# Performance work log

Hardware: AMD Instinct MI355X
Metric: run time of the kernel (lower is better)

Reference implementation:

```python
import jax, jax.numpy as jnp
import numpy as np

B, L, H, HD, FD = 1, 1024, 32, 64, 64
HID = H * HD
EPS = 1e-12


def setup_inputs() -> dict:
    key = jax.random.key(0)
    ks = jax.random.split(key, 7)
    s = 1.0 / np.sqrt(HID)
    return {
        "hidden_states": jax.random.normal(ks[0], (B, L, HID), dtype=jnp.float32),
        "Wq": jax.random.normal(ks[1], (HID, HID), dtype=jnp.float32) * s,
        "Wk": jax.random.normal(ks[2], (HID, HID), dtype=jnp.float32) * s,
        "Wv": jax.random.normal(ks[3], (HID, HID), dtype=jnp.float32) * s,
        "Wo": jax.random.normal(ks[4], (HID, HID), dtype=jnp.float32) * s,
        "Wfq": jax.random.normal(ks[5], (H, HD, FD), dtype=jnp.float32) * (1.0 / np.sqrt(HD)),
        "Wfk": jax.random.normal(ks[6], (H, HD, FD), dtype=jnp.float32) * (1.0 / np.sqrt(HD)),
    }


def _heads(x):
    # [b, l, hid] -> [b, h, l, hd]
    b, l, _ = x.shape
    return x.reshape(b, l, H, HD).transpose(0, 2, 1, 3)


def _feature_map(x, Wf):
    # per-head learned kernel + softmax over feature dim (hedgehog-style)
    z = jnp.einsum('bhld,hdf->bhlf', x, Wf)
    return jax.nn.softmax(z, axis=-1)


def _linear_attention(q, k, v, eps=EPS):
    # causal_dot_product: cumsum of outer-product KV state (fp32)
    qf, kf, vf = q.astype(jnp.float32), k.astype(jnp.float32), v.astype(jnp.float32)
    kv = jnp.cumsum(jnp.einsum('bhlf,bhld->bhlfd', kf, vf), axis=2)  # [b,h,l,f,d]
    y = jnp.einsum('bhlf,bhlfd->bhld', qf, kv)
    # fp32_attention=False branch: normalizer computed on cumsum(k)
    k_cum = jnp.cumsum(kf, axis=2).astype(q.dtype)
    denom = jnp.einsum('bhld,bhld->bhl', q, k_cum) + eps
    return y.astype(q.dtype) / denom[..., None]


def reference(hidden_states, Wq, Wk, Wv, Wo, Wfq, Wfk):
    b, l, _ = hidden_states.shape
    q = _heads(hidden_states @ Wq.T)
    k = _heads(hidden_states @ Wk.T)
    v = _heads(hidden_states @ Wv.T)
    fq = _feature_map(q, Wfq)
    fk = _feature_map(k, Wfk)
    y = _linear_attention(fq, fk, v)  # [b,h,l,hd]
    y = y.transpose(0, 2, 1, 3).reshape(b, l, HID)
    return y @ Wo.T
```

## Files before the change

kernel.cpp:

```cpp
#include <hip/hip_runtime.h>
#include <math.h>

constexpr int LQ  = 1024;
constexpr int NH  = 32;
constexpr int HDM = 64;
constexpr int FDM = 64;
constexpr int HID = 2048;
constexpr int NCH = 16;
constexpr int CT  = 64;
#define EPSV 1e-12f

typedef __bf16 bf16x8 __attribute__((ext_vector_type(8)));
typedef float  f32x4  __attribute__((ext_vector_type(4)));

__device__ __forceinline__ unsigned short f2b_raw(float x) {
    union { float f; unsigned int u; } v; v.f = x;
    unsigned int r = v.u + 0x7fffu + ((v.u >> 16) & 1u);
    return (unsigned short)(r >> 16);
}
__device__ __forceinline__ float b2f(ushort u) {
    union { unsigned int i; float f; } v; v.i = ((unsigned int)u) << 16; return v.f;
}

#define ASYNC16(ldsp, gp) __builtin_amdgcn_global_load_lds( \
    (const __attribute__((address_space(1))) void*)(gp),    \
    (__attribute__((address_space(3))) void*)(ldsp), 16, 0, 0)

template <int TM, int TN, bool BF16OUT>
__device__ __forceinline__ void gemm_core(const ushort* __restrict__ A,
                                          const ushort* __restrict__ B,
                                          void* __restrict__ Cv,
                                          int M, int N, int K) {
    constexpr int FI = TM / 32, FJ = TN / 32;
    constexpr int AI = TM / 32, BJ = TN / 32;
    constexpr int ASZ = TM * 64, BSZ = TN * 64;
    __shared__ __align__(16) ushort As[2 * ASZ];
    __shared__ __align__(16) ushort Bs[2 * BSZ];

    const int t = threadIdx.x, wave = t >> 6, lane = t & 63;
    const int wr = (wave >> 1) * (TM / 2), wc = (wave & 1) * (TN / 2);
    const int bm = blockIdx.y * TM, bn = blockIdx.x * TN;

    const int grow = lane >> 3;
    const int gsw  = ((lane & 7) ^ (grow & 7)) << 3;
    const int arow0 = wave * (TM / 4), brow0 = wave * (TN / 4);
    const ushort* gA = A + (size_t)(bm + arow0 + grow) * K + gsw;
    const ushort* gB = B + (size_t)(bn + brow0 + grow) * K + gsw;

    const int fr = lane & 15, q = lane >> 4;

    f32x4 acc[FI][FJ] = {};
    const int NIT = K >> 6;

    {
        ushort* ab = As + arow0 * 64;
        ushort* bb = Bs + brow0 * 64;
#pragma unroll
        for (int i = 0; i < AI; ++i) ASYNC16(ab + i * 512, gA + (size_t)i * 8 * K);
#pragma unroll
        for (int j = 0; j < BJ; ++j) ASYNC16(bb + j * 512, gB + (size_t)j * 8 * K);
    }
    __syncthreads();

    for (int it = 0; it < NIT; ++it) {
        const int p = it & 1;
        if (it + 1 < NIT) {
            const int ko = (it + 1) << 6;
            ushort* ab = As + (p ^ 1) * ASZ + arow0 * 64;
            ushort* bb = Bs + (p ^ 1) * BSZ + brow0 * 64;
#pragma unroll
            for (int i = 0; i < AI; ++i) ASYNC16(ab + i * 512, gA + ko + (size_t)i * 8 * K);
#pragma unroll
            for (int j = 0; j < BJ; ++j) ASYNC16(bb + j * 512, gB + ko + (size_t)j * 8 * K);
        }
        const ushort* ap = As + p * ASZ;
        const ushort* bp = Bs + p * BSZ;
        bf16x8 af[2][FI], bg[2][FJ];
#pragma unroll
        for (int ks = 0; ks < 2; ++ks) {
#pragma unroll
            for (int i = 0; i < FI; ++i) {
                const int row = wr + i * 16 + fr;
                af[ks][i] = *(const bf16x8*)&ap[row * 64 + (((q + ks * 4) ^ (row & 7)) << 3)];
            }
#pragma unroll
            for (int j = 0; j < FJ; ++j) {
                const int row = wc + j * 16 + fr;
                bg[ks][j] = *(const bf16x8*)&bp[row * 64 + (((q + ks * 4) ^ (row & 7)) << 3)];
            }
        }
#pragma unroll
        for (int ks = 0; ks < 2; ++ks)
#pragma unroll
            for (int i = 0; i < FI; ++i)
#pragma unroll
                for (int j = 0; j < FJ; ++j)
                    acc[i][j] = __builtin_amdgcn_mfma_f32_16x16x32_bf16(af[ks][i], bg[ks][j], acc[i][j], 0, 0, 0);
        if (it + 1 < NIT) __syncthreads();
    }

    const int er = q * 4, ec = lane & 15;
#pragma unroll
    for (int i = 0; i < FI; ++i)
#pragma unroll
        for (int j = 0; j < FJ; ++j) {
            const size_t base = (size_t)(bm + wr + i * 16 + er) * N + bn + wc + j * 16 + ec;
            if constexpr (BF16OUT) {
                ushort* C = (ushort*)Cv;
#pragma unroll
                for (int r = 0; r < 4; ++r) C[base + (size_t)r * N] = f2b_raw(acc[i][j][r]);
            } else {
                float* C = (float*)Cv;
#pragma unroll
                for (int r = 0; r < 4; ++r) C[base + (size_t)r * N] = acc[i][j][r];
            }
        }
}

__global__ __launch_bounds__(256) void gemm_one(const ushort* __restrict__ A,
                                                const ushort* __restrict__ B,
                                                float* __restrict__ C) {
    gemm_core<64, 64, false>(A, B, C, LQ, HID, HID);
}

__global__ __launch_bounds__(256) void gemm_qkv_fm(
    const ushort* __restrict__ hsb,
    const ushort* __restrict__ wqb, const ushort* __restrict__ wkb,
    const ushort* __restrict__ wvb,
    const ushort* __restrict__ WfqT, const ushort* __restrict__ WfkT,
    ushort* __restrict__ fqB, ushort* __restrict__ fkB,
    ushort* __restrict__ VTb) {
    constexpr int TM = 64, TN = 128;
    constexpr int ASZ = TM * 64, BSZ = TN * 64;
    __shared__ __align__(16) ushort lds[2 * ASZ + 2 * BSZ];
    ushort* As = lds;
    ushort* Bs = lds + 2 * ASZ;

    const int z = blockIdx.z;
    const ushort* Bmat = (z == 0) ? wqb : (z == 1) ? wkb : wvb;

    const int t = threadIdx.x, wave = t >> 6, lane = t & 63;
    const int wr = (wave >> 1) * 32, wc = (wave & 1) * 64;
    const int bx = blockIdx.x, c = blockIdx.y;
    const int bm = c * TM, bn = bx * TN, l0 = c * CT;

    const int grow = lane >> 3;
    const int gsw  = ((lane & 7) ^ (grow & 7)) << 3;
    const int arow0 = wave * 16, brow0 = wave * 32;
    const ushort* gA = hsb  + (size_t)(bm + arow0 + grow) * HID + gsw;
    const ushort* gB = Bmat + (size_t)(bn + brow0 + grow) * HID + gsw;

    const int fr = lane & 15, q = lane >> 4, ec = lane & 15;

    f32x4 acc[2][4] = {};
    const int NIT = HID >> 6;

    {
        ushort* ab = As + arow0 * 64;
        ushort* bb = Bs + brow0 * 64;
#pragma unroll
        for (int i = 0; i < 2; ++i) ASYNC16(ab + i * 512, gA + (size_t)i * 8 * HID);
#pragma unroll
        for (int j = 0; j < 4; ++j) ASYNC16(bb + j * 512, gB + (size_t)j * 8 * HID);
    }
    __syncthreads();

    for (int it = 0; it < NIT; ++it) {
        const int p = it & 1;
        if (it + 1 < NIT) {
            const int ko = (it + 1) << 6;
            ushort* ab = As + (p ^ 1) * ASZ + arow0 * 64;
            ushort* bb = Bs + (p ^ 1) * BSZ + brow0 * 64;
#pragma unroll
            for (int i = 0; i < 2; ++i) ASYNC16(ab + i * 512, gA + ko + (size_t)i * 8 * HID);
#pragma unroll
            for (int j = 0; j < 4; ++j) ASYNC16(bb + j * 512, gB + ko + (size_t)j * 8 * HID);
        }
        const ushort* ap = As + p * ASZ;
        const ushort* bp = Bs + p * BSZ;
        bf16x8 af[2][2], bg[2][4];
#pragma unroll
        for (int ks = 0; ks < 2; ++ks) {
#pragma unroll
            for (int i = 0; i < 2; ++i) {
                const int row = wr + i * 16 + fr;
                af[ks][i] = *(const bf16x8*)&ap[row * 64 + (((q + ks * 4) ^ (row & 7)) << 3)];
            }
#pragma unroll
            for (int j = 0; j < 4; ++j) {
                const int row = wc + j * 16 + fr;
                bg[ks][j] = *(const bf16x8*)&bp[row * 64 + (((q + ks * 4) ^ (row & 7)) << 3)];
            }
        }
#pragma unroll
        for (int ks = 0; ks < 2; ++ks)
#pragma unroll
            for (int i = 0; i < 2; ++i)
#pragma unroll
                for (int j = 0; j < 4; ++j)
                    acc[i][j] = __builtin_amdgcn_mfma_f32_16x16x32_bf16(af[ks][i], bg[ks][j], acc[i][j], 0, 0, 0);
        if (it + 1 < NIT) __syncthreads();
    }

    if (z == 2) {
#pragma unroll
        for (int i = 0; i < 2; ++i)
#pragma unroll
            for (int j = 0; j < 4; ++j) {
                const int col = wc + j * 16 + ec;
                const int hh = col >> 6, d = col & 63;
                const int lb = wr + i * 16 + q * 4;
                const size_t base = (((size_t)(2 * bx + hh) * NCH + c) * 64 + d) * 64 + lb;
                ushort4 o = make_ushort4(f2b_raw(acc[i][j][0]), f2b_raw(acc[i][j][1]),
                                         f2b_raw(acc[i][j][2]), f2b_raw(acc[i][j][3]));
                *(ushort4*)&VTb[base] = o;
            }
        return;
    }

    __syncthreads();
    ushort* Qt  = lds;
    ushort* Wfs = lds + 8704;
#pragma unroll
    for (int i = 0; i < 2; ++i)
#pragma unroll
        for (int j = 0; j < 4; ++j)
#pragma unroll
            for (int r = 0; r < 4; ++r)
                Qt[(wr + i * 16 + q * 4 + r) * 136 + wc + j * 16 + ec] = f2b_raw(acc[i][j][r]);
    {
        const ushort* WT = ((z == 0) ? WfqT : WfkT) + (size_t)(2 * bx) * 4096;
#pragma unroll
        for (int it = 0; it < 4; ++it) {
            const int e = it * 2048 + t * 8;
            const int hh = e >> 12, f = (e >> 6) & 63, dc = e & 63;
            uint4 wv4 = *(const uint4*)&WT[e];
            *(uint4*)&Wfs[hh * 4608 + f * 72 + dc] = wv4;
        }
    }
    __syncthreads();

    const int hh = wave & 1, R0 = (wave >> 1) * 32;
    f32x4 z2[2][4] = {};
#pragma unroll
    for (int ks = 0; ks < 2; ++ks) {
        bf16x8 a[2];
#pragma unroll
        for (int i = 0; i < 2; ++i)
            a[i] = *(const bf16x8*)&Qt[(R0 + i * 16 + fr) * 136 + hh * 64 + ks * 32 + q * 8];
#pragma unroll
        for (int j = 0; j < 4; ++j) {
            bf16x8 b = *(const bf16x8*)&Wfs[hh * 4608 + (j * 16 + fr) * 72 + ks * 32 + q * 8];
#pragma unroll
            for (int i = 0; i < 2; ++i)
                z2[i][j] = __builtin_amdgcn_mfma_f32_16x16x32_bf16(a[i], b, z2[i][j], 0, 0, 0);
        }
    }

    ushort* outp = (z == 0) ? fqB : fkB;
    const int hgl = 2 * bx + hh;
#pragma unroll
    for (int i = 0; i < 2; ++i)
#pragma unroll
        for (int r = 0; r < 4; ++r) {
            float m = z2[i][0][r];
#pragma unroll
            for (int j = 1; j < 4; ++j) m = fmaxf(m, z2[i][j][r]);
            m = fmaxf(m, __shfl_xor(m, 1)); m = fmaxf(m, __shfl_xor(m, 2));
            m = fmaxf(m, __shfl_xor(m, 4)); m = fmaxf(m, __shfl_xor(m, 8));
            float e4[4], s = 0.f;
#pragma unroll
            for (int j = 0; j < 4; ++j) { e4[j] = __expf(z2[i][j][r] - m); s += e4[j]; }
            s += __shfl_xor(s, 1); s += __shfl_xor(s, 2);
            s += __shfl_xor(s, 4); s += __shfl_xor(s, 8);
            const float inv = 1.0f / s;
            const int l = R0 + i * 16 + q * 4 + r;
            ushort* op = outp + ((size_t)hgl * LQ + l0 + l) * FDM;
#pragma unroll
            for (int j = 0; j < 4; ++j) op[j * 16 + ec] = f2b_raw(e4[j] * inv);
        }
}

struct ConvArgs {
    const float* src[5]; ushort* dst[5]; int n[5];
    const float* Wfq; const float* Wfk; ushort* WfqT; ushort* WfkT;
};
__global__ __launch_bounds__(256) void conv_all(ConvArgs p) {
    const int y = blockIdx.y, t = threadIdx.x;
    if (y < 5) {
        const int i = (blockIdx.x * 256 + t) * 4;
        if (i >= p.n[y]) return;
        float4 v = *(const float4*)&p.src[y][i];
        ushort4 o = make_ushort4(f2b_raw(v.x), f2b_raw(v.y), f2b_raw(v.z), f2b_raw(v.w));
        *(ushort4*)&p.dst[y][i] = o;
        return;
    }
    if (blockIdx.x >= NH) return;
    const int h = blockIdx.x;
    const float* src = ((y == 6) ? p.Wfk : p.Wfq) + (size_t)h * 4096;
    ushort* dst = ((y == 6) ? p.WfkT : p.WfqT) + (size_t)h * 4096;
    __shared__ float tile[64][65];
    for (int it = 0; it < 16; ++it) {
        int e = it * 256 + t; int d = e >> 6, f = e & 63;
        tile[d][f] = src[e];
    }
    __syncthreads();
    for (int it = 0; it < 16; ++it) {
        int e = it * 256 + t; int f = e >> 6, d = e & 63;
        dst[e] = f2b_raw(tile[d][f]);
    }
}

__global__ __launch_bounds__(256) void chunk_state(
    const ushort* __restrict__ fkB, const ushort* __restrict__ VTb,
    float* __restrict__ Sraw, float* __restrict__ Ks) {
    __shared__ __align__(16) ushort Vs[64 * 72];
    __shared__ __align__(16) ushort Fs[64 * 72];
    const int c = blockIdx.x, h = blockIdx.y;
    const int t = threadIdx.x, lane = t & 63, w = t >> 6;
    const int l0 = c * CT;
    const int fr = lane & 15, q = lane >> 4, ec = lane & 15;
    const size_t cb = ((size_t)h * NCH + c) * 4096;

    for (int it = 0; it < 2; ++it) {
        const int e = (it * 256 + t) * 8;
        const int row = e >> 6, col = e & 63;
        *(uint4*)&Vs[row * 72 + col] = *(const uint4*)&VTb[cb + e];
        uint4 fv = *(const uint4*)&fkB[((size_t)h * LQ + l0) * FDM + e];
        const ushort* pf = (const ushort*)&fv;
#pragma unroll
        for (int i2 = 0; i2 < 8; ++i2) Fs[(col + i2) * 72 + row] = pf[i2];
    }
    __syncthreads();

    f32x4 acc[4] = {};
#pragma unroll
    for (int ks = 0; ks < 2; ++ks) {
        bf16x8 a = *(const bf16x8*)&Vs[(w * 16 + fr) * 72 + ks * 32 + q * 8];
#pragma unroll
        for (int j = 0; j < 4; ++j) {
            bf16x8 b = *(const bf16x8*)&Fs[(j * 16 + fr) * 72 + ks * 32 + q * 8];
            acc[j] = __builtin_amdgcn_mfma_f32_16x16x32_bf16(a, b, acc[j], 0, 0, 0);
        }
    }
    float* sp = Sraw + cb;
#pragma unroll
    for (int j = 0; j < 4; ++j)
#pragma unroll
        for (int r = 0; r < 4; ++r)
            sp[(w * 16 + q * 4 + r) * 64 + j * 16 + ec] = acc[j][r];
    if (t < 64) {
        float s = 0.f;
#pragma unroll 8
        for (int l = 0; l < 64; ++l) s += b2f(Fs[t * 72 + l]);
        Ks[((size_t)h * NCH + c) * FDM + t] = s;
    }
}

__global__ __launch_bounds__(256) void prefix2(const float* __restrict__ Sraw,
                                               ushort* __restrict__ SpreB,
                                               const float* __restrict__ Ks,
                                               float* __restrict__ Kpre) {
    const int h = blockIdx.x, eb = blockIdx.y, t = threadIdx.x;
    const int e0 = eb * 512 + t * 2;
    float r0 = 0.f, r1 = 0.f;
    const size_t hb = (size_t)h * NCH * 4096;
    for (int c2 = 0; c2 < NCH; ++c2) {
        const size_t base = hb + (size_t)c2 * 4096 + e0;
        float c0 = Sraw[base], c1 = Sraw[base + 1];
        ushort2 o = make_ushort2(f2b_raw(r0), f2b_raw(r1));
        *(ushort2*)&SpreB[base] = o;
        r0 += c0; r1 += c1;
    }
    if (eb == 0 && t < 64) {
        float rk = 0.f;
        for (int c2 = 0; c2 < NCH; ++c2) {
            const size_t kb2 = ((size_t)h * NCH + c2) * FDM + t;
            float cur = Ks[kb2];
            Kpre[kb2] = rk;
            rk += cur;
        }
    }
}

__global__ __launch_bounds__(256) void intra2(
    const ushort* __restrict__ fqB, const ushort* __restrict__ fkB,
    const ushort* __restrict__ VTb, const ushort* __restrict__ SpreB,
    const float* __restrict__ Kpre, ushort* __restrict__ Yb) {
    __shared__ __align__(16) ushort fqs[64 * 72];
    __shared__ __align__(16) ushort fks[64 * 72];
    __shared__ __align__(16) ushort VTs[64 * 72];
    __shared__ __align__(16) ushort Sps[64 * 72];
    __shared__ __align__(16) ushort Pms[64 * 72];
    __shared__ float den[64], kpr[64];

    const int c = blockIdx.x, h = blockIdx.y;
    const int t = threadIdx.x, lane = t & 63, wave = t >> 6;
    const int l0 = c * CT;
    const int fr = lane & 15, fo = (lane >> 4) * 8;
    const int g = lane >> 4, cc = lane & 15;

    const size_t qkbase = ((size_t)h * LQ + l0) * FDM;
    const size_t cbase  = ((size_t)h * NCH + c) * 4096;
    for (int it = 0; it < 2; ++it) {
        int e = (it * 256 + t) * 8;
        int row = e >> 6, col = e & 63;
        *(uint4*)&fqs[row * 72 + col] = *(const uint4*)&fqB[qkbase + e];
        *(uint4*)&fks[row * 72 + col] = *(const uint4*)&fkB[qkbase + e];
        *(uint4*)&VTs[row * 72 + col] = *(const uint4*)&VTb[cbase + e];
        *(uint4*)&Sps[row * 72 + col] = *(const uint4*)&SpreB[cbase + e];
    }
    if (t < 64) kpr[t] = Kpre[((size_t)h * NCH + c) * FDM + t];
    __syncthreads();

    f32x4 accP[4] = {};
#pragma unroll
    for (int kp = 0; kp < 2; ++kp) {
        bf16x8 a = *(const bf16x8*)&fqs[(wave * 16 + fr) * 72 + kp * 32 + fo];
#pragma unroll
        for (int j = 0; j < 4; ++j) {
            bf16x8 b = *(const bf16x8*)&fks[(j * 16 + fr) * 72 + kp * 32 + fo];
            accP[j] = __builtin_amdgcn_mfma_f32_16x16x32_bf16(a, b, accP[j], 0, 0, 0);
        }
    }
#pragma unroll
    for (int j = 0; j < 4; ++j)
#pragma unroll
        for (int r = 0; r < 4; ++r) {
            int l = wave * 16 + g * 4 + r, lp = j * 16 + cc;
            Pms[l * 72 + lp] = (lp <= l) ? f2b_raw(accP[j][r]) : (ushort)0;
        }
    __syncthreads();

    {
        const int srow = t >> 2, spart = t & 3;
        float s = 0.f;
#pragma unroll
        for (int i = 0; i < 16; ++i) s += b2f(Pms[srow * 72 + spart * 16 + i]);
#pragma unroll
        for (int i = 0; i < 16; ++i) s += b2f(fqs[srow * 72 + spart * 16 + i]) * kpr[spart * 16 + i];
        s += __shfl_xor(s, 1); s += __shfl_xor(s, 2);
        if (spart == 0) den[srow] = s + EPSV;
    }
    __syncthreads();

    f32x4 accY[4] = {};
#pragma unroll
    for (int kp = 0; kp < 2; ++kp) {
        bf16x8 a = *(const bf16x8*)&Pms[(wave * 16 + fr) * 72 + kp * 32 + fo];
#pragma unroll
        for (int j = 0; j < 4; ++j) {
            bf16x8 b = *(const bf16x8*)&VTs[(j * 16 + fr) * 72 + kp * 32 + fo];
            accY[j] = __builtin_amdgcn_mfma_f32_16x16x32_bf16(a, b, accY[j], 0, 0, 0);
        }
    }
#pragma unroll
    for (int kp = 0; kp < 2; ++kp) {
        bf16x8 a = *(const bf16x8*)&fqs[(wave * 16 + fr) * 72 + kp * 32 + fo];
#pragma unroll
        for (int j = 0; j < 4; ++j) {
            bf16x8 b = *(const bf16x8*)&Sps[(j * 16 + fr) * 72 + kp * 32 + fo];
            accY[j] = __builtin_amdgcn_mfma_f32_16x16x32_bf16(a, b, accY[j], 0, 0, 0);
        }
    }
#pragma unroll
    for (int r = 0; r < 4; ++r) {
        int l = wave * 16 + g * 4 + r;
        float inv = 1.0f / den[l];
        ushort* yo = Yb + (size_t)(l0 + l) * HID + h * HDM;
#pragma unroll
        for (int j = 0; j < 4; ++j)
            yo[j * 16 + cc] = f2b_raw(accY[j][r] * inv);
    }
}

extern "C" void kernel_launch(void* const* d_in, const int* in_sizes, int n_in,
                              void* d_out, int out_size, void* d_ws, size_t ws_size,
                              hipStream_t stream) {
    const float* hs  = (const float*)d_in[0];
    const float* Wq  = (const float*)d_in[1];
    const float* Wk  = (const float*)d_in[2];
    const float* Wv  = (const float*)d_in[3];
    const float* Wo  = (const float*)d_in[4];
    const float* Wfq = (const float*)d_in[5];
    const float* Wfk = (const float*)d_in[6];
    float* out = (float*)d_out;

    const size_t SZ = (size_t)LQ * HID;
    const size_t WZ = (size_t)HID * HID;

    char* w = (char*)d_ws;
    auto aus = [&](size_t n) { ushort* p = (ushort*)w; w += n * sizeof(ushort); return p; };
    auto afl = [&](size_t n) { float*  p = (float*)w;  w += n * sizeof(float);  return p; };

    ushort* hsb   = aus(SZ);
    ushort* wqb   = aus(WZ);
    ushort* wkb   = aus(WZ);
    ushort* wvb   = aus(WZ);
    ushort* wob   = aus(WZ);
    ushort* fqB   = aus(SZ);
    ushort* fkB   = aus(SZ);
    ushort* VTb   = aus(SZ);
    ushort* WfqT  = aus((size_t)NH * 4096);
    ushort* WfkT  = aus((size_t)NH * 4096);
    ushort* SpreB = aus(SZ);
    ushort* Yb    = aus(SZ);
    float*  Sraw  = afl(SZ);
    float*  Ks    = afl((size_t)NH * NCH * FDM);
    float*  Kpre  = afl((size_t)NH * NCH * FDM);

    ConvArgs ca;
    ca.src[0] = hs; ca.dst[0] = hsb; ca.n[0] = (int)SZ;
    ca.src[1] = Wq; ca.dst[1] = wqb; ca.n[1] = (int)WZ;
    ca.src[2] = Wk; ca.dst[2] = wkb; ca.n[2] = (int)WZ;
    ca.src[3] = Wv; ca.dst[3] = wvb; ca.n[3] = (int)WZ;
    ca.src[4] = Wo; ca.dst[4] = wob; ca.n[4] = (int)WZ;
    ca.Wfq = Wfq; ca.Wfk = Wfk; ca.WfqT = WfqT; ca.WfkT = WfkT;
    conv_all<<<dim3((unsigned)(WZ / 1024), 7), 256, 0, stream>>>(ca);

    gemm_qkv_fm<<<dim3(HID / 128, LQ / 64, 3), 256, 0, stream>>>(
        hsb, wqb, wkb, wvb, WfqT, WfkT, fqB, fkB, VTb);

    chunk_state<<<dim3(NCH, NH), 256, 0, stream>>>(fkB, VTb, Sraw, Ks);

    prefix2<<<dim3(NH, 8), 256, 0, stream>>>(Sraw, SpreB, Ks, Kpre);

    intra2<<<dim3(NCH, NH), 256, 0, stream>>>(fqB, fkB, VTb, SpreB, Kpre, Yb);

    gemm_one<<<dim3(HID / 64, LQ / 64), 256, 0, stream>>>(Yb, wob, out);
}
```

Measured before the change: 195.2 us.

## Enlarge GEMM tiles and fuse chunk state with prefix scan

The QKV+feature-map GEMM moves to 128x128 tiles and drops double buffering in favour of a single-buffer load/sync loop. The feature-map step now runs per head in two passes over shared memory. The output GEMM uses wider 64x128 tiles. chunk_state and prefix2 are merged into one state_scan kernel that computes the per-chunk KV outer products with scalar FMAs while keeping the running prefix in registers, so the fp32 Sraw intermediate and one launch go away. The costs are less latency hiding in the GEMM, fewer blocks (lower occupancy), and a scalar, serial state scan in place of MFMA.

After: 259.0 us. +32.7%, slower.

```diff
diff --git a/kernel.cpp b/kernel.cpp
--- a/kernel.cpp
+++ b/kernel.cpp
@@ -120,7 +120,7 @@
 __global__ __launch_bounds__(256) void gemm_one(const ushort* __restrict__ A,
                                                 const ushort* __restrict__ B,
                                                 float* __restrict__ C) {
-    gemm_core<64, 64, false>(A, B, C, LQ, HID, HID);
+    gemm_core<64, 128, false>(A, B, C, LQ, HID, HID);
 }
 
 __global__ __launch_bounds__(256) void gemm_qkv_fm(
@@ -130,87 +130,69 @@
     const ushort* __restrict__ WfqT, const ushort* __restrict__ WfkT,
     ushort* __restrict__ fqB, ushort* __restrict__ fkB,
     ushort* __restrict__ VTb) {
-    constexpr int TM = 64, TN = 128;
-    constexpr int ASZ = TM * 64, BSZ = TN * 64;
-    __shared__ __align__(16) ushort lds[2 * ASZ + 2 * BSZ];
+    __shared__ __align__(16) ushort lds[16384];
     ushort* As = lds;
-    ushort* Bs = lds + 2 * ASZ;
+    ushort* Bs = lds + 8192;
 
     const int z = blockIdx.z;
     const ushort* Bmat = (z == 0) ? wqb : (z == 1) ? wkb : wvb;
 
     const int t = threadIdx.x, wave = t >> 6, lane = t & 63;
-    const int wr = (wave >> 1) * 32, wc = (wave & 1) * 64;
-    const int bx = blockIdx.x, c = blockIdx.y;
-    const int bm = c * TM, bn = bx * TN, l0 = c * CT;
+    const int wr = (wave >> 1) * 64, wc = (wave & 1) * 64;
+    const int bx = blockIdx.x, by = blockIdx.y;
+    const int bm = by * 128, bn = bx * 128;
 
     const int grow = lane >> 3;
     const int gsw  = ((lane & 7) ^ (grow & 7)) << 3;
-    const int arow0 = wave * 16, brow0 = wave * 32;
-    const ushort* gA = hsb  + (size_t)(bm + arow0 + grow) * HID + gsw;
-    const ushort* gB = Bmat + (size_t)(bn + brow0 + grow) * HID + gsw;
+    const ushort* gA = hsb  + (size_t)(bm + wave * 32 + grow) * HID + gsw;
+    const ushort* gB = Bmat + (size_t)(bn + wave * 32 + grow) * HID + gsw;
+    ushort* la = As + (wave * 32) * 64;
+    ushort* lb = Bs + (wave * 32) * 64;
 
     const int fr = lane & 15, q = lane >> 4, ec = lane & 15;
 
-    f32x4 acc[2][4] = {};
-    const int NIT = HID >> 6;
-
-    {
-        ushort* ab = As + arow0 * 64;
-        ushort* bb = Bs + brow0 * 64;
-#pragma unroll
-        for (int i = 0; i < 2; ++i) ASYNC16(ab + i * 512, gA + (size_t)i * 8 * HID);
-#pragma unroll
-        for (int j = 0; j < 4; ++j) ASYNC16(bb + j * 512, gB + (size_t)j * 8 * HID);
-    }
-    __syncthreads();
-
-    for (int it = 0; it < NIT; ++it) {
-        const int p = it & 1;
-        if (it + 1 < NIT) {
-            const int ko = (it + 1) << 6;
-            ushort* ab = As + (p ^ 1) * ASZ + arow0 * 64;
-            ushort* bb = Bs + (p ^ 1) * BSZ + brow0 * 64;
-#pragma unroll
-            for (int i = 0; i < 2; ++i) ASYNC16(ab + i * 512, gA + ko + (size_t)i * 8 * HID);
-#pragma unroll
-            for (int j = 0; j < 4; ++j) ASYNC16(bb + j * 512, gB + ko + (size_t)j * 8 * HID);
-        }
-        const ushort* ap = As + p * ASZ;
-        const ushort* bp = Bs + p * BSZ;
-        bf16x8 af[2][2], bg[2][4];
+    f32x4 acc[4][4] = {};
+
+    for (int k0 = 0; k0 < HID; k0 += 64) {
+        __syncthreads();
+#pragma unroll
+        for (int i = 0; i < 4; ++i) ASYNC16(la + i * 512, gA + k0 + (size_t)i * 8 * HID);
+#pragma unroll
+        for (int j = 0; j < 4; ++j) ASYNC16(lb + j * 512, gB + k0 + (size_t)j * 8 * HID);
+        __syncthreads();
+        bf16x8 af[2][4], bg[2][4];
 #pragma unroll
         for (int ks = 0; ks < 2; ++ks) {
 #pragma unroll
-            for (int i = 0; i < 2; ++i) {
+            for (int i = 0; i < 4; ++i) {
                 const int row = wr + i * 16 + fr;
-                af[ks][i] = *(const bf16x8*)&ap[row * 64 + (((q + ks * 4) ^ (row & 7)) << 3)];
+                af[ks][i] = *(const bf16x8*)&As[row * 64 + (((q + ks * 4) ^ (row & 7)) << 3)];
             }
 #pragma unroll
             for (int j = 0; j < 4; ++j) {
                 const int row = wc + j * 16 + fr;
-                bg[ks][j] = *(const bf16x8*)&bp[row * 64 + (((q + ks * 4) ^ (row & 7)) << 3)];
+                bg[ks][j] = *(const bf16x8*)&Bs[row * 64 + (((q + ks * 4) ^ (row & 7)) << 3)];
             }
         }
 #pragma unroll
         for (int ks = 0; ks < 2; ++ks)
 #pragma unroll
-            for (int i = 0; i < 2; ++i)
+            for (int i = 0; i < 4; ++i)
 #pragma unroll
                 for (int j = 0; j < 4; ++j)
                     acc[i][j] = __builtin_amdgcn_mfma_f32_16x16x32_bf16(af[ks][i], bg[ks][j], acc[i][j], 0, 0, 0);
-        if (it + 1 < NIT) __syncthreads();
     }
 
     if (z == 2) {
 #pragma unroll
-        for (int i = 0; i < 2; ++i)
+        for (int i = 0; i < 4; ++i)
 #pragma unroll
             for (int j = 0; j < 4; ++j) {
-                const int col = wc + j * 16 + ec;
-                const int hh = col >> 6, d = col & 63;
-                const int lb = wr + i * 16 + q * 4;
-                const size_t base = (((size_t)(2 * bx + hh) * NCH + c) * 64 + d) * 64 + lb;
+                const int colL = wc + j * 16 + ec;
+                const int head = 2 * bx + (colL >> 6), d = colL & 63;
+                const int chunk = 2 * by + (wr >> 6);
+                const int lloc = i * 16 + q * 4;
+                const size_t base = (((size_t)head * NCH + chunk) * 64 + d) * 64 + lloc;
                 ushort4 o = make_ushort4(f2b_raw(acc[i][j][0]), f2b_raw(acc[i][j][1]),
                                          f2b_raw(acc[i][j][2]), f2b_raw(acc[i][j][3]));
                 *(ushort4*)&VTb[base] = o;
@@ -218,67 +200,67 @@
         return;
     }
 
-    __syncthreads();
     ushort* Qt  = lds;
-    ushort* Wfs = lds + 8704;
-#pragma unroll
-    for (int i = 0; i < 2; ++i)
-#pragma unroll
-        for (int j = 0; j < 4; ++j)
-#pragma unroll
-            for (int r = 0; r < 4; ++r)
-                Qt[(wr + i * 16 + q * 4 + r) * 136 + wc + j * 16 + ec] = f2b_raw(acc[i][j][r]);
-    {
-        const ushort* WT = ((z == 0) ? WfqT : WfkT) + (size_t)(2 * bx) * 4096;
-#pragma unroll
-        for (int it = 0; it < 4; ++it) {
-            const int e = it * 2048 + t * 8;
-            const int hh = e >> 12, f = (e >> 6) & 63, dc = e & 63;
-            uint4 wv4 = *(const uint4*)&WT[e];
-            *(uint4*)&Wfs[hh * 4608 + f * 72 + dc] = wv4;
-        }
-    }
-    __syncthreads();
-
-    const int hh = wave & 1, R0 = (wave >> 1) * 32;
-    f32x4 z2[2][4] = {};
-#pragma unroll
-    for (int ks = 0; ks < 2; ++ks) {
-        bf16x8 a[2];
+    ushort* Wfs = lds + 9728;
+    ushort* outp = (z == 0) ? fqB : fkB;
+
+    for (int hp = 0; hp < 2; ++hp) {
+        __syncthreads();
+        if ((wave & 1) == hp) {
+#pragma unroll
+            for (int i = 0; i < 4; ++i)
+#pragma unroll
+                for (int j = 0; j < 4; ++j)
+#pragma unroll
+                    for (int r = 0; r < 4; ++r)
+                        Qt[(wr + i * 16 + q * 4 + r) * 72 + j * 16 + ec] = f2b_raw(acc[i][j][r]);
+        }
+        const int hgl = 2 * bx + hp;
+        {
+            const ushort* WT = ((z == 0) ? WfqT : WfkT) + (size_t)hgl * 4096;
+            const int e = t * 16, f = e >> 6, dc = e & 63;
+            *(uint4*)&Wfs[f * 72 + dc]     = *(const uint4*)&WT[e];
+            *(uint4*)&Wfs[f * 72 + dc + 8] = *(const uint4*)&WT[e + 8];
+        }
+        __syncthreads();
+
+        const int R0 = wave * 32;
+        f32x4 zf[2][4] = {};
+#pragma unroll
+        for (int ks = 0; ks < 2; ++ks) {
+            bf16x8 a[2];
+#pragma unroll
+            for (int i = 0; i < 2; ++i)
+                a[i] = *(const bf16x8*)&Qt[(R0 + i * 16 + fr) * 72 + ks * 32 + q * 8];
+#pragma unroll
+            for (int j = 0; j < 4; ++j) {
+                bf16x8 b = *(const bf16x8*)&Wfs[(j * 16 + fr) * 72 + ks * 32 + q * 8];
+#pragma unroll
+                for (int i = 0; i < 2; ++i)
+                    zf[i][j] = __builtin_amdgcn_mfma_f32_16x16x32_bf16(a[i], b, zf[i][j], 0, 0, 0);
+            }
+        }
 #pragma unroll
         for (int i = 0; i < 2; ++i)
-            a[i] = *(const bf16x8*)&Qt[(R0 + i * 16 + fr) * 136 + hh * 64 + ks * 32 + q * 8];
-#pragma unroll
-        for (int j = 0; j < 4; ++j) {
-            bf16x8 b = *(const bf16x8*)&Wfs[hh * 4608 + (j * 16 + fr) * 72 + ks * 32 + q * 8];
-#pragma unroll
-            for (int i = 0; i < 2; ++i)
-                z2[i][j] = __builtin_amdgcn_mfma_f32_16x16x32_bf16(a[i], b, z2[i][j], 0, 0, 0);
-        }
-    }
-
-    ushort* outp = (z == 0) ? fqB : fkB;
-    const int hgl = 2 * bx + hh;
-#pragma unroll
-    for (int i = 0; i < 2; ++i)
-#pragma unroll
-        for (int r = 0; r < 4; ++r) {
-            float m = z2[i][0][r];
-#pragma unroll
-            for (int j = 1; j < 4; ++j) m = fmaxf(m, z2[i][j][r]);
-            m = fmaxf(m, __shfl_xor(m, 1)); m = fmaxf(m, __shfl_xor(m, 2));
-            m = fmaxf(m, __shfl_xor(m, 4)); m = fmaxf(m, __shfl_xor(m, 8));
-            float e4[4], s = 0.f;
-#pragma unroll
-            for (int j = 0; j < 4; ++j) { e4[j] = __expf(z2[i][j][r] - m); s += e4[j]; }
-            s += __shfl_xor(s, 1); s += __shfl_xor(s, 2);
-            s += __shfl_xor(s, 4); s += __shfl_xor(s, 8);
-            const float inv = 1.0f / s;
-            const int l = R0 + i * 16 + q * 4 + r;
-            ushort* op = outp + ((size_t)hgl * LQ + l0 + l) * FDM;
-#pragma unroll
-            for (int j = 0; j < 4; ++j) op[j * 16 + ec] = f2b_raw(e4[j] * inv);
-        }
+#pragma unroll
+            for (int r = 0; r < 4; ++r) {
+                float m = zf[i][0][r];
+#pragma unroll
+                for (int j = 1; j < 4; ++j) m = fmaxf(m, zf[i][j][r]);
+                m = fmaxf(m, __shfl_xor(m, 1)); m = fmaxf(m, __shfl_xor(m, 2));
+                m = fmaxf(m, __shfl_xor(m, 4)); m = fmaxf(m, __shfl_xor(m, 8));
+                float e4[4], s = 0.f;
+#pragma unroll
+                for (int j = 0; j < 4; ++j) { e4[j] = __expf(zf[i][j][r] - m); s += e4[j]; }
+                s += __shfl_xor(s, 1); s += __shfl_xor(s, 2);
+                s += __shfl_xor(s, 4); s += __shfl_xor(s, 8);
+                const float inv = 1.0f / s;
+                const int l = bm + R0 + i * 16 + q * 4 + r;
+                ushort* op = outp + ((size_t)hgl * LQ + l) * FDM;
+#pragma unroll
+                for (int j = 0; j < 4; ++j) op[j * 16 + ec] = f2b_raw(e4[j] * inv);
+            }
+    }
 }
 
 struct ConvArgs {
@@ -311,74 +293,46 @@
     }
 }
 
-__global__ __launch_bounds__(256) void chunk_state(
+__global__ __launch_bounds__(256) void state_scan(
     const ushort* __restrict__ fkB, const ushort* __restrict__ VTb,
-    float* __restrict__ Sraw, float* __restrict__ Ks) {
-    __shared__ __align__(16) ushort Vs[64 * 72];
-    __shared__ __align__(16) ushort Fs[64 * 72];
-    const int c = blockIdx.x, h = blockIdx.y;
-    const int t = threadIdx.x, lane = t & 63, w = t >> 6;
-    const int l0 = c * CT;
-    const int fr = lane & 15, q = lane >> 4, ec = lane & 15;
-    const size_t cb = ((size_t)h * NCH + c) * 4096;
-
-    for (int it = 0; it < 2; ++it) {
-        const int e = (it * 256 + t) * 8;
-        const int row = e >> 6, col = e & 63;
-        *(uint4*)&Vs[row * 72 + col] = *(const uint4*)&VTb[cb + e];
-        uint4 fv = *(const uint4*)&fkB[((size_t)h * LQ + l0) * FDM + e];
-        const ushort* pf = (const ushort*)&fv;
-#pragma unroll
-        for (int i2 = 0; i2 < 8; ++i2) Fs[(col + i2) * 72 + row] = pf[i2];
-    }
-    __syncthreads();
-
-    f32x4 acc[4] = {};
-#pragma unroll
-    for (int ks = 0; ks < 2; ++ks) {
-        bf16x8 a = *(const bf16x8*)&Vs[(w * 16 + fr) * 72 + ks * 32 + q * 8];
-#pragma unroll
-        for (int j = 0; j < 4; ++j) {
-            bf16x8 b = *(const bf16x8*)&Fs[(j * 16 + fr) * 72 + ks * 32 + q * 8];
-            acc[j] = __builtin_amdgcn_mfma_f32_16x16x32_bf16(a, b, acc[j], 0, 0, 0);
-        }
-    }
-    float* sp = Sraw + cb;
-#pragma unroll
-    for (int j = 0; j < 4; ++j)
-#pragma unroll
-        for (int r = 0; r < 4; ++r)
-            sp[(w * 16 + q * 4 + r) * 64 + j * 16 + ec] = acc[j][r];
-    if (t < 64) {
-        float s = 0.f;
+    ushort* __restrict__ SpreB, float* __restrict__ Kpre) {
+    __shared__ __align__(16) ushort fks[64 * 64];
+    __shared__ __align__(16) ushort vts[8 * 64];
+    const int h = blockIdx.x, eb = blockIdx.y, t = threadIdx.x;
+    const int dr0 = eb * 8;
+    const int dloc = t >> 5, f = (t * 2) & 63;
+    float run0 = 0.f, run1 = 0.f, rk = 0.f;
+
+    for (int c = 0; c < NCH; ++c) {
+        __syncthreads();
+        {
+            const int e = t * 16;
+            const size_t fb = ((size_t)h * LQ + c * CT) * FDM;
+            *(uint4*)&fks[e]     = *(const uint4*)&fkB[fb + e];
+            *(uint4*)&fks[e + 8] = *(const uint4*)&fkB[fb + e + 8];
+            if (t < 64) {
+                const size_t vb = (((size_t)h * NCH + c) * 64 + dr0) * 64;
+                *(uint4*)&vts[t * 8] = *(const uint4*)&VTb[vb + t * 8];
+            }
+        }
+        __syncthreads();
+
+        const size_t sbase = ((size_t)h * NCH + c) * 4096 + dr0 * 64 + t * 2;
+        ushort2 pr = make_ushort2(f2b_raw(run0), f2b_raw(run1));
+        *(ushort2*)&SpreB[sbase] = pr;
+
 #pragma unroll 8
-        for (int l = 0; l < 64; ++l) s += b2f(Fs[t * 72 + l]);
-        Ks[((size_t)h * NCH + c) * FDM + t] = s;
-    }
-}
-
-__global__ __launch_bounds__(256) void prefix2(const float* __restrict__ Sraw,
-                                               ushort* __restrict__ SpreB,
-                                               const float* __restrict__ Ks,
-                                               float* __restrict__ Kpre) {
-    const int h = blockIdx.x, eb = blockIdx.y, t = threadIdx.x;
-    const int e0 = eb * 512 + t * 2;
-    float r0 = 0.f, r1 = 0.f;
-    const size_t hb = (size_t)h * NCH * 4096;
-    for (int c2 = 0; c2 < NCH; ++c2) {
-        const size_t base = hb + (size_t)c2 * 4096 + e0;
-        float c0 = Sraw[base], c1 = Sraw[base + 1];
-        ushort2 o = make_ushort2(f2b_raw(r0), f2b_raw(r1));
-        *(ushort2*)&SpreB[base] = o;
-        r0 += c0; r1 += c1;
-    }
-    if (eb == 0 && t < 64) {
-        float rk = 0.f;
-        for (int c2 = 0; c2 < NCH; ++c2) {
-            const size_t kb2 = ((size_t)h * NCH + c2) * FDM + t;
-            float cur = Ks[kb2];
-            Kpre[kb2] = rk;
-            rk += cur;
+        for (int l = 0; l < 64; ++l) {
+            const float vt = b2f(vts[dloc * 64 + l]);
+            run0 += vt * b2f(fks[l * 64 + f]);
+            run1 += vt * b2f(fks[l * 64 + f + 1]);
+        }
+        if (eb == 0 && t < 64) {
+            Kpre[((size_t)h * NCH + c) * FDM + t] = rk;
+            float s = 0.f;
+#pragma unroll 8
+            for (int l = 0; l < 64; ++l) s += b2f(fks[l * 64 + t]);
+            rk += s;
         }
     }
 }
@@ -505,8 +459,6 @@
     ushort* WfkT  = aus((size_t)NH * 4096);
     ushort* SpreB = aus(SZ);
     ushort* Yb    = aus(SZ);
-    float*  Sraw  = afl(SZ);
-    float*  Ks    = afl((size_t)NH * NCH * FDM);
     float*  Kpre  = afl((size_t)NH * NCH * FDM);
 
     ConvArgs ca;
@@ -518,14 +470,12 @@
     ca.Wfq = Wfq; ca.Wfk = Wfk; ca.WfqT = WfqT; ca.WfkT = WfkT;
     conv_all<<<dim3((unsigned)(WZ / 1024), 7), 256, 0, stream>>>(ca);
 
-    gemm_qkv_fm<<<dim3(HID / 128, LQ / 64, 3), 256, 0, stream>>>(
+    gemm_qkv_fm<<<dim3(HID / 128, LQ / 128, 3), 256, 0, stream>>>(
         hsb, wqb, wkb, wvb, WfqT, WfkT, fqB, fkB, VTb);
 
-    chunk_state<<<dim3(NCH, NH), 256, 0, stream>>>(fkB, VTb, Sraw, Ks);
-
-    prefix2<<<dim3(NH, 8), 256, 0, stream>>>(Sraw, SpreB, Ks, Kpre);
+    state_scan<<<dim3(NH, 8), 256, 0, stream>>>(fkB, VTb, SpreB, Kpre);
 
     intra2<<<dim3(NCH, NH), 256, 0, stream>>>(fqB, fkB, VTb, SpreB, Kpre, Yb);
 
-    gemm_one<<<dim3(HID / 64, LQ / 64), 256, 0, stream>>>(Yb, wob, out);
-}
+    gemm_one<<<dim3(HID / 128, LQ / 64), 256, 0, stream>>>(Yb, wob, out);
+}
```
